# Kernel optimization log

Hardware: AMD Instinct MI355X
Metric: run time of the kernel (lower is better)

Reference implementation:

```python
import jax, jax.numpy as jnp
import numpy as np

DIM = 512
HEADS = 8
HEAD_DIM = DIM // HEADS
SCALE = HEAD_DIM ** -0.5
B, H, W = 8, 64, 64


def rotate_every_two(x):
    # interleaved pair rotation: (x0,x1,x2,x3,...) -> (-x1,x0,-x3,x2,...)
    x1 = x[..., ::2]
    x2 = x[..., 1::2]
    return jnp.stack([-x2, x1], axis=-1).reshape(x.shape)


def theta_shift(x, sin, cos):
    return x * cos + rotate_every_two(x) * sin


def setup_inputs() -> dict:
    key = jax.random.key(0)
    ks = jax.random.split(key, 6)
    N = H * W
    x = jax.random.normal(ks[0], (B, DIM, H, W), jnp.float32)
    sin = jax.random.uniform(ks[1], (N, HEAD_DIM), jnp.float32, minval=-1.0, maxval=1.0)
    cos = jax.random.uniform(ks[2], (N, HEAD_DIM), jnp.float32, minval=-1.0, maxval=1.0)
    w_qkvo = jax.random.normal(ks[3], (4 * DIM, DIM), jnp.float32) * (DIM ** -0.5)
    b_qkvo = jnp.zeros((4 * DIM,), jnp.float32)
    w_lepe = jax.random.normal(ks[4], (DIM, 1, 5, 5), jnp.float32) * 0.1
    b_lepe = jnp.zeros((DIM,), jnp.float32)
    w_proj = jax.random.normal(ks[5], (DIM, DIM), jnp.float32) * (DIM ** -0.5)
    b_proj = jnp.zeros((DIM,), jnp.float32)
    return dict(x=x, sin=sin, cos=cos, w_qkvo=w_qkvo, b_qkvo=b_qkvo,
                w_lepe=w_lepe, b_lepe=b_lepe, w_proj=w_proj, b_proj=b_proj)


def reference(x, sin, cos, w_qkvo, b_qkvo, w_lepe, b_lepe, w_proj, b_proj):
    Bx, C, Hx, Wx = x.shape
    N = Hx * Wx
    # 1x1 conv qkvo projection
    qkvo = jnp.einsum('bchw,oc->bohw', x, w_qkvo) + b_qkvo[None, :, None, None]
    qkv = qkvo[:, :3 * DIM]
    o = qkvo[:, 3 * DIM:]
    # depthwise 5x5 lepe on v (spatial layout)
    v_sp = qkv[:, 2 * DIM:3 * DIM]
    lepe = jax.lax.conv_general_dilated(
        v_sp, w_lepe, window_strides=(1, 1), padding=((2, 2), (2, 2)),
        dimension_numbers=('NCHW', 'OIHW', 'NCHW'), feature_group_count=DIM,
    ) + b_lepe[None, :, None, None]
    # b (3 n d) h w -> (3, b, n, N, d)
    qkv5 = qkv.reshape(Bx, 3, HEADS, HEAD_DIM, N).transpose(1, 0, 2, 4, 3)
    q, k, v = qkv5[0], qkv5[1], qkv5[2]
    q = jax.nn.elu(q) + 1.0
    k = jax.nn.elu(k) + 1.0
    # softmax-gated eff weighting of k
    q_mean = q.mean(axis=-2, keepdims=True)                       # (b,n,1,d)
    eff = SCALE * jnp.einsum('bnod,bntd->bnot', q_mean, k)        # (b,n,1,N)
    eff = jax.nn.softmax(eff, axis=-1).swapaxes(-1, -2)           # (b,n,N,1)
    k = k * eff * N
    # RoPE-style rotation
    q_rope = theta_shift(q, sin, cos)
    k_rope = theta_shift(k, sin, cos)
    # normalizer z (uses un-rotated q, gated k)
    z = 1.0 / (jnp.einsum('bntd,bnod->bnto', q, k.mean(axis=-2, keepdims=True)) + 1e-6)  # (b,n,N,1)
    # linear-attention kv accumulation (d x d)
    inv_sqrt_n = N ** -0.5
    kv = jnp.einsum('bntd,bnte->bnde', k_rope * inv_sqrt_n, v * inv_sqrt_n)  # (b,n,d,d)
    res = jnp.einsum('bntd,bnde->bnte', q_rope, kv) * z            # (b,n,N,d)
    # b n N d -> b (n d) h w
    res = res.transpose(0, 1, 3, 2).reshape(Bx, DIM, Hx, Wx)
    res = res + lepe
    out = jnp.einsum('bchw,oc->bohw', res * o, w_proj) + b_proj[None, :, None, None]
    return out
```

## Files before the change

### kernel.cpp

```cpp
#include <hip/hip_runtime.h>
#include <math.h>

#define N_SP 4096
#define DIMC 512
#define HEADS 8
#define HD 64
#define CH_STRIDE 1536

typedef __attribute__((ext_vector_type(8))) short short8;
typedef __attribute__((ext_vector_type(4))) float f32x4;

__device__ __forceinline__ float elu1(float x) { return x > 0.f ? x + 1.f : expf(x); }

__device__ __forceinline__ float waveSum(float v) {
#pragma unroll
    for (int o = 1; o < 64; o <<= 1) v += __shfl_xor(v, o);
    return v;
}
__device__ __forceinline__ float waveMax(float v) {
#pragma unroll
    for (int o = 1; o < 64; o <<= 1) v = fmaxf(v, __shfl_xor(v, o));
    return v;
}

__device__ __forceinline__ unsigned short f2bf(float f) {
    union { float f; unsigned u; } v; v.f = f;
    unsigned r = v.u + 0x7fffu + ((v.u >> 16) & 1u);
    return (unsigned short)(r >> 16);
}
__device__ __forceinline__ unsigned pk2(float lo, float hi) {
    return (unsigned)f2bf(lo) | ((unsigned)f2bf(hi) << 16);
}

template<bool GATED>
__global__ __launch_bounds__(256) void gemm_bf16(
    const float* __restrict__ W, const float* __restrict__ bias,
    const float* __restrict__ Bsrc, const float* __restrict__ Gsrc,
    float* __restrict__ C, int src_cstride, int dst_cstride)
{
    __shared__ unsigned short Ws[4096];
    __shared__ unsigned short Xs[4096];
    int b  = blockIdx.z;
    int bo = blockIdx.y * 128;
    int bn = blockIdx.x * 128;
    const float* Bb = Bsrc + (size_t)b * src_cstride * N_SP + bn;
    const float* Gb = GATED ? (Gsrc + (size_t)b * src_cstride * N_SP + bn) : nullptr;
    int tid  = threadIdx.x;
    int lane = tid & 63;
    int wid  = tid >> 6;
    int wm = (wid >> 1) * 64, wn = (wid & 1) * 64;
    int quad = lane >> 4, l16 = lane & 15;
    int sm = tid >> 1, sp = tid & 1;
    int xn = tid & 127, xk0 = tid >> 7;

    f32x4 acc[4][4];
#pragma unroll
    for (int i = 0; i < 4; i++)
#pragma unroll
        for (int j = 0; j < 4; j++) acc[i][j] = f32x4{0.f, 0.f, 0.f, 0.f};

    for (int c0 = 0; c0 < DIMC; c0 += 32) {
        const float* wp = W + (size_t)(bo + sm) * DIMC + c0 + sp * 16;
        float4 w0 = *(const float4*)(wp);
        float4 w1 = *(const float4*)(wp + 4);
        float4 w2 = *(const float4*)(wp + 8);
        float4 w3 = *(const float4*)(wp + 12);
        float xv[2][8];
#pragma unroll
        for (int g = 0; g < 2; g++) {
            int kb = xk0 + g * 2;
            const float* xp = Bb + (size_t)(c0 + kb * 8) * N_SP + xn;
#pragma unroll
            for (int i = 0; i < 8; i++) xv[g][i] = xp[(size_t)i * N_SP];
            if (GATED) {
                const float* gp = Gb + (size_t)(c0 + kb * 8) * N_SP + xn;
#pragma unroll
                for (int i = 0; i < 8; i++) xv[g][i] *= gp[(size_t)i * N_SP];
            }
        }
        if (c0) __syncthreads();
        {
            uint4 a, bq;
            a.x  = pk2(w0.x, w0.y); a.y  = pk2(w0.z, w0.w);
            a.z  = pk2(w1.x, w1.y); a.w  = pk2(w1.z, w1.w);
            bq.x = pk2(w2.x, w2.y); bq.y = pk2(w2.z, w2.w);
            bq.z = pk2(w3.x, w3.y); bq.w = pk2(w3.z, w3.w);
            *(uint4*)&Ws[(2 * sp)     * 1024 + sm * 8] = a;
            *(uint4*)&Ws[(2 * sp + 1) * 1024 + sm * 8] = bq;
        }
#pragma unroll
        for (int g = 0; g < 2; g++) {
            int kb = xk0 + g * 2;
            uint4 a;
            a.x = pk2(xv[g][0], xv[g][1]); a.y = pk2(xv[g][2], xv[g][3]);
            a.z = pk2(xv[g][4], xv[g][5]); a.w = pk2(xv[g][6], xv[g][7]);
            *(uint4*)&Xs[kb * 1024 + xn * 8] = a;
        }
        __syncthreads();
        short8 af[4], bf[4];
#pragma unroll
        for (int i = 0; i < 4; i++) {
            af[i] = *(const short8*)&Ws[quad * 1024 + (wm + i * 16 + l16) * 8];
            bf[i] = *(const short8*)&Xs[quad * 1024 + (wn + i * 16 + l16) * 8];
        }
#pragma unroll
        for (int i = 0; i < 4; i++)
#pragma unroll
            for (int j = 0; j < 4; j++)
                acc[i][j] = __builtin_amdgcn_mfma_f32_16x16x32_bf16(
                    af[i], bf[j], acc[i][j], 0, 0, 0);
    }
    float* Cb = C + (size_t)b * dst_cstride * N_SP;
#pragma unroll
    for (int i = 0; i < 4; i++) {
        int row0 = bo + wm + i * 16 + quad * 4;
#pragma unroll
        for (int r = 0; r < 4; r++) {
            float bi = bias[row0 + r];
            float* cr = Cb + (size_t)(row0 + r) * N_SP + bn + wn + l16;
#pragma unroll
            for (int j = 0; j < 4; j++)
                cr[j * 16] = acc[i][j][r] + bi;
        }
    }
}

__global__ __launch_bounds__(256) void qmean_kernel(
    const float* __restrict__ QKV, float* __restrict__ qmean)
{
    int d = blockIdx.x, h = blockIdx.y, b = blockIdx.z;
    const float* row = QKV + ((size_t)b * CH_STRIDE + h * 64 + d) * N_SP;
    int tid = threadIdx.x;
    float s = 0.f;
#pragma unroll
    for (int j = 0; j < 4; j++) {
        float4 v = ((const float4*)row)[j * 256 + tid];
        s += elu1(v.x) + elu1(v.y) + elu1(v.z) + elu1(v.w);
    }
    s = waveSum(s);
    __shared__ float red[4];
    if ((tid & 63) == 0) red[tid >> 6] = s;
    __syncthreads();
    if (tid == 0)
        qmean[((size_t)b * 8 + h) * 64 + d] = (red[0] + red[1] + red[2] + red[3]) * (1.f / N_SP);
}

__global__ __launch_bounds__(256) void logits_kernel(
    const float* __restrict__ QKV, const float* __restrict__ qmean,
    float* __restrict__ eff)
{
    int tc = blockIdx.x, h = blockIdx.y, b = blockIdx.z;
    int tid = threadIdx.x;
    int t = tc * 256 + tid;
    __shared__ float qm[64];
    if (tid < 64) qm[tid] = qmean[((size_t)b * 8 + h) * 64 + tid];
    __syncthreads();
    const float* kb = QKV + ((size_t)b * CH_STRIDE + 512 + h * 64) * N_SP;
    float s = 0.f;
#pragma unroll 8
    for (int d = 0; d < 64; d++) s += qm[d] * elu1(kb[(size_t)d * N_SP + t]);
    eff[((size_t)b * 8 + h) * N_SP + t] = 0.125f * s;
}

__global__ __launch_bounds__(256) void softmax_kernel(float* __restrict__ eff)
{
    int bh = blockIdx.x;
    float* row = eff + (size_t)bh * N_SP;
    int tid = threadIdx.x;
    float4 v[4];
#pragma unroll
    for (int j = 0; j < 4; j++) v[j] = ((float4*)row)[j * 256 + tid];
    float m = -1e30f;
#pragma unroll
    for (int j = 0; j < 4; j++)
        m = fmaxf(m, fmaxf(fmaxf(v[j].x, v[j].y), fmaxf(v[j].z, v[j].w)));
    m = waveMax(m);
    __shared__ float red[8];
    if ((tid & 63) == 0) red[tid >> 6] = m;
    __syncthreads();
    m = fmaxf(fmaxf(red[0], red[1]), fmaxf(red[2], red[3]));
    float s = 0.f;
#pragma unroll
    for (int j = 0; j < 4; j++) {
        v[j].x = expf(v[j].x - m); v[j].y = expf(v[j].y - m);
        v[j].z = expf(v[j].z - m); v[j].w = expf(v[j].w - m);
        s += v[j].x + v[j].y + v[j].z + v[j].w;
    }
    float ws = waveSum(s);
    if ((tid & 63) == 0) red[4 + (tid >> 6)] = ws;
    __syncthreads();
    float tot = red[4] + red[5] + red[6] + red[7];
    float sc = (float)N_SP / tot;
#pragma unroll
    for (int j = 0; j < 4; j++) {
        v[j].x *= sc; v[j].y *= sc; v[j].z *= sc; v[j].w *= sc;
        ((float4*)row)[j * 256 + tid] = v[j];
    }
}

__global__ __launch_bounds__(256) void kv_kernel(
    const float* __restrict__ QKV, const float* __restrict__ eff,
    const float* __restrict__ sinp, const float* __restrict__ cosp,
    float* __restrict__ kv, float* __restrict__ kmean)
{
    int sp = blockIdx.x;
    int h = blockIdx.y, b = blockIdx.z;
    int bh = b * 8 + h;
    int tid = threadIdx.x;
    int r = tid >> 2, quad = tid & 3;
    const float* krow = QKV + ((size_t)b * CH_STRIDE + 512 + h * 64 + r) * N_SP;
    const float* vrow = QKV + ((size_t)b * CH_STRIDE + 1024 + h * 64 + r) * N_SP;
    const float* prow = eff + (size_t)bh * N_SP;
    __shared__ float ksr[64 * 65];
    __shared__ float vs[64 * 65];
    int dg = tid >> 4, eg = tid & 15;
    float acc[4][4];
#pragma unroll
    for (int i = 0; i < 4; i++)
#pragma unroll
        for (int j = 0; j < 4; j++) acc[i][j] = 0.f;
    float km = 0.f;
    float sgn = (r & 1) ? 1.f : -1.f;

    for (int c = 0; c < 8; c++) {
        int t0 = sp * 512 + c * 64;
        int tb = t0 + quad * 16;
        float kx[16], vv[16];
#pragma unroll
        for (int i4 = 0; i4 < 4; i4++) {
            float4 kf = *(const float4*)(krow + tb + i4 * 4);
            float4 pf = *(const float4*)(prow + tb + i4 * 4);
            float4 vf = *(const float4*)(vrow + tb + i4 * 4);
            kx[i4 * 4 + 0] = elu1(kf.x) * pf.x;
            kx[i4 * 4 + 1] = elu1(kf.y) * pf.y;
            kx[i4 * 4 + 2] = elu1(kf.z) * pf.z;
            kx[i4 * 4 + 3] = elu1(kf.w) * pf.w;
            vv[i4 * 4 + 0] = vf.x; vv[i4 * 4 + 1] = vf.y;
            vv[i4 * 4 + 2] = vf.z; vv[i4 * 4 + 3] = vf.w;
        }
#pragma unroll
        for (int i = 0; i < 16; i++) km += kx[i];
        __syncthreads();
#pragma unroll
        for (int i = 0; i < 16; i++) {
            float partner = __shfl_xor(kx[i], 4);
            int t = tb + i;
            float sv = sinp[(size_t)t * 64 + r];
            float cv = cosp[(size_t)t * 64 + r];
            float kr = kx[i] * cv + sgn * partner * sv;
            ksr[r * 65 + (t - t0)] = kr;
            vs[r * 65 + (t - t0)] = vv[i];
        }
        __syncthreads();
#pragma unroll 8
        for (int t = 0; t < 64; t++) {
            float a[4], bb[4];
#pragma unroll
            for (int i = 0; i < 4; i++) a[i] = ksr[(dg * 4 + i) * 65 + t];
#pragma unroll
            for (int j = 0; j < 4; j++) bb[j] = vs[(eg * 4 + j) * 65 + t];
#pragma unroll
            for (int i = 0; i < 4; i++)
#pragma unroll
                for (int j = 0; j < 4; j++) acc[i][j] += a[i] * bb[j];
        }
    }
#pragma unroll
    for (int i = 0; i < 4; i++)
#pragma unroll
        for (int j = 0; j < 4; j++)
            atomicAdd(&kv[((size_t)bh * 64 + dg * 4 + i) * 64 + eg * 4 + j],
                      acc[i][j] * (1.f / N_SP));
    km += __shfl_xor(km, 1);
    km += __shfl_xor(km, 2);
    if (quad == 0) atomicAdd(&kmean[(size_t)bh * 64 + r], km * (1.f / N_SP));
}

__global__ __launch_bounds__(256) void res_kernel(
    const float* __restrict__ QKV, const float* __restrict__ kv,
    const float* __restrict__ kmean,
    const float* __restrict__ sinp, const float* __restrict__ cosp,
    float* __restrict__ res)
{
    int tc = blockIdx.x;
    int h = blockIdx.y, b = blockIdx.z;
    int bh = b * 8 + h;
    int tid = threadIdx.x;
    int t0 = tc * 64;
    __shared__ float qsr[64 * 65];
    __shared__ float qse[64 * 65];
    __shared__ float kvs[64 * 65];
    __shared__ float zs[64];
    __shared__ float kms[64];
#pragma unroll
    for (int j = 0; j < 16; j++) {
        int lin = j * 256 + tid;
        kvs[(lin >> 6) * 65 + (lin & 63)] = kv[(size_t)bh * 4096 + lin];
    }
    if (tid < 64) kms[tid] = kmean[(size_t)bh * 64 + tid];

    int r = tid >> 2, quad = tid & 3;
    const float* qrow = QKV + ((size_t)b * CH_STRIDE + h * 64 + r) * N_SP;
    float sgn = (r & 1) ? 1.f : -1.f;
    int tb = t0 + quad * 16;
#pragma unroll
    for (int i4 = 0; i4 < 4; i4++) {
        float4 qf = *(const float4*)(qrow + tb + i4 * 4);
        float qe[4] = { elu1(qf.x), elu1(qf.y), elu1(qf.z), elu1(qf.w) };
#pragma unroll
        for (int ii = 0; ii < 4; ii++) {
            float partner = __shfl_xor(qe[ii], 4);
            int t = tb + i4 * 4 + ii;
            float sv = sinp[(size_t)t * 64 + r];
            float cv = cosp[(size_t)t * 64 + r];
            qse[r * 65 + (t - t0)] = qe[ii];
            qsr[r * 65 + (t - t0)] = qe[ii] * cv + sgn * partner * sv;
        }
    }
    __syncthreads();
    if (tid < 64) {
        float s = 0.f;
#pragma unroll 8
        for (int d = 0; d < 64; d++) s += qse[d * 65 + tid] * kms[d];
        zs[tid] = 1.f / (s + 1e-6f);
    }
    __syncthreads();

    int eg = tid >> 4, tg = tid & 15;
    float acc[4][4];
#pragma unroll
    for (int j = 0; j < 4; j++)
#pragma unroll
        for (int i = 0; i < 4; i++) acc[j][i] = 0.f;
#pragma unroll 4
    for (int d = 0; d < 64; d++) {
        float qv[4], kvv[4];
#pragma unroll
        for (int i = 0; i < 4; i++) qv[i] = qsr[d * 65 + tg * 4 + i];
#pragma unroll
        for (int j = 0; j < 4; j++) kvv[j] = kvs[d * 65 + eg * 4 + j];
#pragma unroll
        for (int j = 0; j < 4; j++)
#pragma unroll
            for (int i = 0; i < 4; i++) acc[j][i] += kvv[j] * qv[i];
    }
    float* rb = res + ((size_t)b * CH_STRIDE + 512 + h * 64) * N_SP;
#pragma unroll
    for (int j = 0; j < 4; j++) {
        float4 o4;
        o4.x = acc[j][0] * zs[tg * 4 + 0];
        o4.y = acc[j][1] * zs[tg * 4 + 1];
        o4.z = acc[j][2] * zs[tg * 4 + 2];
        o4.w = acc[j][3] * zs[tg * 4 + 3];
        *(float4*)(rb + (size_t)(eg * 4 + j) * N_SP + t0 + tg * 4) = o4;
    }
}

#define LPS 73
__global__ __launch_bounds__(256) void lepe_kernel(
    const float* __restrict__ QKV, const float* __restrict__ wl,
    const float* __restrict__ bl, float* __restrict__ res)
{
    int c = blockIdx.x & 511;
    int b = blockIdx.x >> 9;
    __shared__ float img[68 * LPS];
    int tid = threadIdx.x;
    const float* vb = QKV + ((size_t)b * CH_STRIDE + 1024 + c) * N_SP;

    for (int i = tid; i < 68 * LPS; i += 256) img[i] = 0.f;
    __syncthreads();
#pragma unroll
    for (int i = 0; i < 4; i++) {
        int p = i * 256 + tid;
        float4 v4 = ((const float4*)vb)[p];
        int y = p >> 4;
        int x = (p & 15) * 4;
        float* dst = &img[(y + 2) * LPS + (x + 2)];
        dst[0] = v4.x; dst[1] = v4.y; dst[2] = v4.z; dst[3] = v4.w;
    }
    float w[25];
    const float* wc = wl + c * 25;
#pragma unroll
    for (int i = 0; i < 25; i++) w[i] = wc[i];
    float bias = bl[c];
    __syncthreads();

    int y  = tid >> 2;
    int x0 = (tid & 3) * 16;
    float acc[16];
#pragma unroll
    for (int u = 0; u < 16; u++) acc[u] = bias;
#pragma unroll
    for (int i = 0; i < 5; i++) {
        float rowv[20];
#pragma unroll
        for (int q = 0; q < 20; q++)
            rowv[q] = img[(y + i) * LPS + x0 + q];
#pragma unroll
        for (int j = 0; j < 5; j++)
#pragma unroll
            for (int u = 0; u < 16; u++)
                acc[u] += rowv[u + j] * w[i * 5 + j];
    }
    float* rr = res + ((size_t)b * CH_STRIDE + 512 + c) * N_SP + y * 64 + x0;
#pragma unroll
    for (int q = 0; q < 4; q++) {
        float4 r4 = *(const float4*)&rr[q * 4];
        r4.x += acc[q * 4 + 0]; r4.y += acc[q * 4 + 1];
        r4.z += acc[q * 4 + 2]; r4.w += acc[q * 4 + 3];
        *(float4*)&rr[q * 4] = r4;
    }
}

extern "C" void kernel_launch(void* const* d_in, const int* in_sizes, int n_in,
                              void* d_out, int out_size, void* d_ws, size_t ws_size,
                              hipStream_t stream)
{
    const float* x      = (const float*)d_in[0];
    const float* sinp   = (const float*)d_in[1];
    const float* cosp   = (const float*)d_in[2];
    const float* w_qkvo = (const float*)d_in[3];
    const float* b_qkvo = (const float*)d_in[4];
    const float* w_lepe = (const float*)d_in[5];
    const float* b_lepe = (const float*)d_in[6];
    const float* w_proj = (const float*)d_in[7];
    const float* b_proj = (const float*)d_in[8];
    float* out = (float*)d_out;
    float* ws  = (float*)d_ws;

    float* qkv   = ws;
    float* eff   = ws + 50331648;
    float* qmean = ws + 50593792;
    float* kmean = ws + 50597888;
    float* kv    = ws + 50601984;

    hipMemsetAsync(kmean, 0, (4096 + 262144) * sizeof(float), stream);

    gemm_bf16<false><<<dim3(32, 12, 8), 256, 0, stream>>>(
        w_qkvo, b_qkvo, x, nullptr, qkv, DIMC, CH_STRIDE);
    qmean_kernel<<<dim3(64, 8, 8), 256, 0, stream>>>(qkv, qmean);
    logits_kernel<<<dim3(16, 8, 8), 256, 0, stream>>>(qkv, qmean, eff);
    softmax_kernel<<<64, 256, 0, stream>>>(eff);
    kv_kernel<<<dim3(8, 8, 8), 256, 0, stream>>>(qkv, eff, sinp, cosp, kv, kmean);
    res_kernel<<<dim3(64, 8, 8), 256, 0, stream>>>(qkv, kv, kmean, sinp, cosp, qkv);
    lepe_kernel<<<4096, 256, 0, stream>>>(qkv, w_lepe, b_lepe, qkv);
    gemm_bf16<false><<<dim3(32, 4, 8), 256, 0, stream>>>(
        w_qkvo + 1536 * DIMC, b_qkvo + 1536, x, nullptr, qkv, DIMC, CH_STRIDE);
    gemm_bf16<true><<<dim3(32, 4, 8), 256, 0, stream>>>(
        w_proj, b_proj, qkv + (size_t)512 * N_SP, qkv, out, CH_STRIDE, DIMC);
}
```

Measured before the change: 570.7 us.

## Pre-convert GEMM operands to transposed bf16 and load via direct-to-LDS loads

```diff
diff --git a/kernel.cpp b/kernel.cpp
--- a/kernel.cpp
+++ b/kernel.cpp
@@ -32,26 +32,105 @@
     return (unsigned)f2bf(lo) | ((unsigned)f2bf(hi) << 16);
 }
 
-template<bool GATED>
-__global__ __launch_bounds__(256) void gemm_bf16(
-    const float* __restrict__ W, const float* __restrict__ bias,
-    const float* __restrict__ Bsrc, const float* __restrict__ Gsrc,
-    float* __restrict__ C, int src_cstride, int dst_cstride)
+__device__ __forceinline__ void gload16(const unsigned short* g, unsigned short* l) {
+    __builtin_amdgcn_global_load_lds(
+        (const __attribute__((address_space(1))) unsigned int*)g,
+        (__attribute__((address_space(3))) unsigned int*)l, 16, 0, 0);
+}
+
+__global__ __launch_bounds__(256) void convert_bf16(
+    const float* __restrict__ src, unsigned short* __restrict__ dst, int n4)
+{
+    int i = blockIdx.x * 256 + threadIdx.x;
+    if (i < n4) {
+        float4 v = ((const float4*)src)[i];
+        uint2 u; u.x = pk2(v.x, v.y); u.y = pk2(v.z, v.w);
+        ((uint2*)dst)[i] = u;
+    }
+}
+
+__global__ __launch_bounds__(256) void transpose_x(
+    const float* __restrict__ X, unsigned short* __restrict__ XT)
+{
+    int ntile = blockIdx.x;
+    int ctile = blockIdx.y;
+    int b     = blockIdx.z;
+    __shared__ float tile[64 * 65];
+    int tid = threadIdx.x;
+    int tr = tid >> 4;
+    int tc = (tid & 15) * 4;
+    const float* xb = X + ((size_t)b * DIMC + ctile * 64) * N_SP + ntile * 64;
+#pragma unroll
+    for (int i = 0; i < 4; i++) {
+        int c = tr + i * 16;
+        float4 v = *(const float4*)(xb + (size_t)c * N_SP + tc);
+        float* d = &tile[c * 65 + tc];
+        d[0] = v.x; d[1] = v.y; d[2] = v.z; d[3] = v.w;
+    }
+    __syncthreads();
+    unsigned short* xt = XT + ((size_t)b * N_SP + ntile * 64) * DIMC + ctile * 64;
+#pragma unroll
+    for (int i = 0; i < 4; i++) {
+        int n = tr + i * 16;
+        uint2 u;
+        u.x = pk2(tile[(tc + 0) * 65 + n], tile[(tc + 1) * 65 + n]);
+        u.y = pk2(tile[(tc + 2) * 65 + n], tile[(tc + 3) * 65 + n]);
+        *(uint2*)(xt + (size_t)n * DIMC + tc) = u;
+    }
+}
+
+__global__ __launch_bounds__(256) void gate_transpose(float* __restrict__ qkv)
+{
+    int ntile = blockIdx.x;
+    int ctile = blockIdx.y;
+    int b     = blockIdx.z;
+    __shared__ float tile[64 * 65];
+    int tid = threadIdx.x;
+    int tr = tid >> 4;
+    int tc = (tid & 15) * 4;
+    const float* rb = qkv + ((size_t)b * CH_STRIDE + 512 + ctile * 64) * N_SP + ntile * 64;
+    const float* ob = qkv + ((size_t)b * CH_STRIDE +       ctile * 64) * N_SP + ntile * 64;
+#pragma unroll
+    for (int i = 0; i < 4; i++) {
+        int c = tr + i * 16;
+        float4 r4 = *(const float4*)(rb + (size_t)c * N_SP + tc);
+        float4 o4 = *(const float4*)(ob + (size_t)c * N_SP + tc);
+        float* d = &tile[c * 65 + tc];
+        d[0] = r4.x * o4.x; d[1] = r4.y * o4.y;
+        d[2] = r4.z * o4.z; d[3] = r4.w * o4.w;
+    }
+    __syncthreads();
+    unsigned short* gt = (unsigned short*)(qkv + ((size_t)b * CH_STRIDE + 1024) * N_SP)
+                         + (size_t)(ntile * 64) * DIMC + ctile * 64;
+#pragma unroll
+    for (int i = 0; i < 4; i++) {
+        int n = tr + i * 16;
+        uint2 u;
+        u.x = pk2(tile[(tc + 0) * 65 + n], tile[(tc + 1) * 65 + n]);
+        u.y = pk2(tile[(tc + 2) * 65 + n], tile[(tc + 3) * 65 + n]);
+        *(uint2*)(gt + (size_t)n * DIMC + tc) = u;
+    }
+}
+
+__global__ __launch_bounds__(256) void gemm_bf16_fast(
+    const unsigned short* __restrict__ A, const float* __restrict__ bias,
+    const unsigned short* __restrict__ B, size_t bstride,
+    float* __restrict__ C, int dst_cstride)
 {
     __shared__ unsigned short Ws[4096];
     __shared__ unsigned short Xs[4096];
     int b  = blockIdx.z;
     int bo = blockIdx.y * 128;
     int bn = blockIdx.x * 128;
-    const float* Bb = Bsrc + (size_t)b * src_cstride * N_SP + bn;
-    const float* Gb = GATED ? (Gsrc + (size_t)b * src_cstride * N_SP + bn) : nullptr;
+    const unsigned short* Ab = A + (size_t)bo * DIMC;
+    const unsigned short* Bb = B + (size_t)b * bstride + (size_t)bn * DIMC;
     int tid  = threadIdx.x;
     int lane = tid & 63;
     int wid  = tid >> 6;
     int wm = (wid >> 1) * 64, wn = (wid & 1) * 64;
     int quad = lane >> 4, l16 = lane & 15;
-    int sm = tid >> 1, sp = tid & 1;
-    int xn = tid & 127, xk0 = tid >> 7;
+    int r0  = tid & 127;
+    int kb0 = tid >> 7;
 
     f32x4 acc[4][4];
 #pragma unroll
@@ -60,42 +139,11 @@
         for (int j = 0; j < 4; j++) acc[i][j] = f32x4{0.f, 0.f, 0.f, 0.f};
 
     for (int c0 = 0; c0 < DIMC; c0 += 32) {
-        const float* wp = W + (size_t)(bo + sm) * DIMC + c0 + sp * 16;
-        float4 w0 = *(const float4*)(wp);
-        float4 w1 = *(const float4*)(wp + 4);
-        float4 w2 = *(const float4*)(wp + 8);
-        float4 w3 = *(const float4*)(wp + 12);
-        float xv[2][8];
-#pragma unroll
-        for (int g = 0; g < 2; g++) {
-            int kb = xk0 + g * 2;
-            const float* xp = Bb + (size_t)(c0 + kb * 8) * N_SP + xn;
-#pragma unroll
-            for (int i = 0; i < 8; i++) xv[g][i] = xp[(size_t)i * N_SP];
-            if (GATED) {
-                const float* gp = Gb + (size_t)(c0 + kb * 8) * N_SP + xn;
-#pragma unroll
-                for (int i = 0; i < 8; i++) xv[g][i] *= gp[(size_t)i * N_SP];
-            }
-        }
         if (c0) __syncthreads();
-        {
-            uint4 a, bq;
-            a.x  = pk2(w0.x, w0.y); a.y  = pk2(w0.z, w0.w);
-            a.z  = pk2(w1.x, w1.y); a.w  = pk2(w1.z, w1.w);
-            bq.x = pk2(w2.x, w2.y); bq.y = pk2(w2.z, w2.w);
-            bq.z = pk2(w3.x, w3.y); bq.w = pk2(w3.z, w3.w);
-            *(uint4*)&Ws[(2 * sp)     * 1024 + sm * 8] = a;
-            *(uint4*)&Ws[(2 * sp + 1) * 1024 + sm * 8] = bq;
-        }
-#pragma unroll
-        for (int g = 0; g < 2; g++) {
-            int kb = xk0 + g * 2;
-            uint4 a;
-            a.x = pk2(xv[g][0], xv[g][1]); a.y = pk2(xv[g][2], xv[g][3]);
-            a.z = pk2(xv[g][4], xv[g][5]); a.w = pk2(xv[g][6], xv[g][7]);
-            *(uint4*)&Xs[kb * 1024 + xn * 8] = a;
-        }
+        gload16(Ab + (size_t)r0 * DIMC + c0 + kb0 * 8,       &Ws[kb0 * 1024 + r0 * 8]);
+        gload16(Ab + (size_t)r0 * DIMC + c0 + (kb0 + 2) * 8, &Ws[(kb0 + 2) * 1024 + r0 * 8]);
+        gload16(Bb + (size_t)r0 * DIMC + c0 + kb0 * 8,       &Xs[kb0 * 1024 + r0 * 8]);
+        gload16(Bb + (size_t)r0 * DIMC + c0 + (kb0 + 2) * 8, &Xs[(kb0 + 2) * 1024 + r0 * 8]);
         __syncthreads();
         short8 af[4], bf[4];
 #pragma unroll
@@ -434,18 +482,34 @@
     float* kmean = ws + 50597888;
     float* kv    = ws + 50601984;
 
+    unsigned short* xT    = (unsigned short*)out;
+    unsigned short* wq_bf = (unsigned short*)out + 16777216;
+    unsigned short* wp_bf = (unsigned short*)kv;
+    unsigned short* gT    = (unsigned short*)(qkv + (size_t)1024 * N_SP);
+
     hipMemsetAsync(kmean, 0, (4096 + 262144) * sizeof(float), stream);
 
-    gemm_bf16<false><<<dim3(32, 12, 8), 256, 0, stream>>>(
-        w_qkvo, b_qkvo, x, nullptr, qkv, DIMC, CH_STRIDE);
+    convert_bf16<<<1024, 256, 0, stream>>>(w_qkvo, wq_bf, 262144);
+    transpose_x<<<dim3(64, 8, 8), 256, 0, stream>>>(x, xT);
+
+    gemm_bf16_fast<<<dim3(32, 12, 8), 256, 0, stream>>>(
+        wq_bf, b_qkvo, xT, (size_t)N_SP * DIMC, qkv, CH_STRIDE);
+
     qmean_kernel<<<dim3(64, 8, 8), 256, 0, stream>>>(qkv, qmean);
     logits_kernel<<<dim3(16, 8, 8), 256, 0, stream>>>(qkv, qmean, eff);
     softmax_kernel<<<64, 256, 0, stream>>>(eff);
     kv_kernel<<<dim3(8, 8, 8), 256, 0, stream>>>(qkv, eff, sinp, cosp, kv, kmean);
     res_kernel<<<dim3(64, 8, 8), 256, 0, stream>>>(qkv, kv, kmean, sinp, cosp, qkv);
+
+    convert_bf16<<<256, 256, 0, stream>>>(w_proj, wp_bf, 65536);
     lepe_kernel<<<4096, 256, 0, stream>>>(qkv, w_lepe, b_lepe, qkv);
-    gemm_bf16<false><<<dim3(32, 4, 8), 256, 0, stream>>>(
-        w_qkvo + 1536 * DIMC, b_qkvo + 1536, x, nullptr, qkv, DIMC, CH_STRIDE);
-    gemm_bf16<true><<<dim3(32, 4, 8), 256, 0, stream>>>(
-        w_proj, b_proj, qkv + (size_t)512 * N_SP, qkv, out, CH_STRIDE, DIMC);
-}
+
+    gemm_bf16_fast<<<dim3(32, 4, 8), 256, 0, stream>>>(
+        wq_bf + (size_t)1536 * DIMC, b_qkvo + 1536, xT, (size_t)N_SP * DIMC,
+        qkv, CH_STRIDE);
+
+    gate_transpose<<<dim3(64, 8, 8), 256, 0, stream>>>(qkv);
+
+    gemm_bf16_fast<<<dim3(32, 4, 8), 256, 0, stream>>>(
+        wp_bf, b_proj, gT, (size_t)CH_STRIDE * N_SP * 2, out, DIMC);
+}
```

Result: no change. 560.3 us (-1.8%).
